# Kernel tuning notes

Hardware: AMD Instinct MI355X
Metric: run time of the kernel (lower is better)

Reference implementation:

```python
import jax, jax.numpy as jnp
import numpy as np

B, L, D, Z, H, N, G = 8, 2048, 1024, 128, 2048, 16, 32
MAXPOS = 2048
EPS = 1e-5
PRIOR_COUNT = 2.0  # TimestepNorm prior pseudo-count


def setup_inputs() -> dict:
    ks = jax.random.split(jax.random.key(0), 12)
    std = 0.02  # bert init
    return {
        "x": jax.random.normal(ks[0], (B, L, D), jnp.float32),
        "prior_mean": jnp.zeros((G,), jnp.float32),
        "prior_logv": jnp.zeros((G,), jnp.float32),
        "tn_weight": jnp.ones((D,), jnp.float32),
        "tn_bias": jnp.zeros((D,), jnp.float32),
        "delta": jax.random.normal(ks[1], (D, N), jnp.float32),
        "alpha": jax.random.normal(ks[2], (D, N), jnp.float32),
        "ema_beta": jax.random.normal(ks[3], (D, N), jnp.float32),
        "ema_gamma": jax.random.normal(ks[4], (D, N), jnp.float32),
        "omega": jax.random.normal(ks[5], (D,), jnp.float32),
        "rms_weight": jnp.ones((D,), jnp.float32),
        "Wv": jax.random.normal(ks[6], (H, D), jnp.float32) * std,
        "bv": jnp.zeros((H,), jnp.float32),
        "Wmx": jax.random.normal(ks[7], (Z + H + 2 * D, D), jnp.float32) * std,
        "bmx": jnp.zeros((Z + H + 2 * D,), jnp.float32),
        "Wh": jax.random.normal(ks[8], (D, H), jnp.float32) * std,
        "qk_gamma": jax.random.normal(ks[9], (2, Z), jnp.float32) * 0.1,
        "qk_beta": jax.random.normal(ks[10], (2, Z), jnp.float32) * 0.1,
        "rel_bias": jax.random.normal(ks[11], (2 * MAXPOS - 1,), jnp.float32) * 0.02,
    }


def timestep_norm(x, prior_mean, prior_logv, weight, bias):
    """Causal cumulative group norm with a prior (TimestepNorm)."""
    m = D // G  # features per group
    xg = x.reshape(B, L, G, m)
    s1 = jnp.cumsum(xg.sum(-1), axis=1)            # B,L,G  running sum
    s2 = jnp.cumsum((xg * xg).sum(-1), axis=1)     # B,L,G  running sum of squares
    cnt = PRIOR_COUNT + m * jnp.arange(1, L + 1, dtype=x.dtype)[None, :, None]
    pv = jnp.exp(prior_logv)
    mean = (PRIOR_COUNT * prior_mean + s1) / cnt
    var = (PRIOR_COUNT * (pv + prior_mean ** 2) + s2) / cnt - mean ** 2
    xn = (xg - mean[..., None]) * jax.lax.rsqrt(var[..., None] + EPS)
    return xn.reshape(B, L, D) * weight + bias


def multihead_ema(x, delta, alpha, ema_beta, ema_gamma, omega):
    """MultiHeadEMA: causal damped-EMA convolution via FFT, plus omega residual."""
    p = jax.nn.sigmoid(delta)                       # D,N
    a = jax.nn.sigmoid(alpha)
    q = 1.0 - p * a                                 # decay in (0,1)
    t = jnp.arange(L, dtype=x.dtype)
    vander = jnp.exp(t[None, None, :] * jnp.log(q)[:, :, None])  # D,N,L
    scale = 1.0 / jnp.sqrt(jnp.asarray(N, x.dtype))
    kern = jnp.einsum('dn,dnl,dn->dl', p * ema_beta, vander, ema_gamma * scale)
    xT = x.transpose(0, 2, 1)                       # B,D,L
    n = 2 * L
    out = jnp.fft.irfft(jnp.fft.rfft(xT, n=n) * jnp.fft.rfft(kern, n=n)[None], n=n)[..., :L]
    out = out + xT * omega[:, None]
    return out.transpose(0, 2, 1)


def _forward(x, prior_mean, prior_logv, tn_weight, tn_bias, delta, alpha,
             ema_beta, ema_gamma, omega, rms_weight, Wv, bv, Wmx, bmx, Wh,
             qk_gamma, qk_beta, rel_bias):
    residual = x
    xn = timestep_norm(x, prior_mean, prior_logv, tn_weight, tn_bias)
    v = jax.nn.silu(xn @ Wv.T + bv)                 # B,L,H
    mx = multihead_ema(xn, delta, alpha, ema_beta, ema_gamma, omega)
    mx = mx * jax.lax.rsqrt(jnp.mean(mx * mx, axis=-1, keepdims=True) + EPS) * rms_weight  # RMSNorm
    base = mx @ Wmx.T + bmx                         # B,L,Z+H+2D
    u = jax.nn.sigmoid(base[..., :D])
    zr = jax.nn.silu(base[..., D:D + Z + H])
    hx = base[..., D + Z + H:]
    z, r = zr[..., :Z], zr[..., Z:]
    zz = z[..., None, :] * qk_gamma + qk_beta       # B,L,2,Z
    q = zz[..., 0, :] * (Z ** -0.5)
    k = zz[..., 1, :]
    # simple relative positional bias: bias[i,j] = rel_bias[MAXPOS-1 + (j-i)]
    idx = (MAXPOS - 1) + (jnp.arange(L)[None, :] - jnp.arange(L)[:, None])
    qk = jnp.einsum('biz,bjz->bij', q, k) + rel_bias[idx]
    causal = jnp.tril(jnp.ones((L, L), bool))
    qk = jnp.where(causal, qk, -jnp.inf)
    attn = jax.nn.softmax(qk, axis=-1)              # B,L,L
    h = jnp.einsum('bij,bjh->bih', attn, v)         # B,L,H
    h = jax.nn.silu(hx + (h * r) @ Wh.T)            # B,L,D
    return residual + u * (h - residual)


def reference(x, prior_mean, prior_logv, tn_weight, tn_bias, delta, alpha,
              ema_beta, ema_gamma, omega, rms_weight, Wv, bv, Wmx, bmx, Wh,
              qk_gamma, qk_beta, rel_bias):
    return _forward(x, prior_mean, prior_logv, tn_weight, tn_bias, delta, alpha,
                    ema_beta, ema_gamma, omega, rms_weight, Wv, bv, Wmx, bmx, Wh,
                    qk_gamma, qk_beta, rel_bias)
```

## Files before the change

kernel.cpp:

```cpp
#include <hip/hip_runtime.h>
#include <stdint.h>

#define B_ 8
#define L_ 2048
#define D_ 1024
#define Z_ 128
#define H_ 2048
#define NE_ 16
#define G_ 32
#define MAXPOS_ 2048
#define NMX_ 4224
#define EPS_ 1e-5f
#define PC_ 2.0f
#define NTILE_ 16
#define NPACK_ 136
#define TILE_ELEMS_ 16384

typedef short bf16x8 __attribute__((ext_vector_type(8)));
typedef float f32x4 __attribute__((ext_vector_type(4)));

__device__ __forceinline__ float bf2f(uint16_t u) {
  union { uint32_t u; float f; } v; v.u = ((uint32_t)u) << 16; return v.f;
}
__device__ __forceinline__ uint16_t f2bf(float f) {
  union { float f; uint32_t u; } v; v.f = f;
  uint32_t r = (v.u + 0x7FFFu + ((v.u >> 16) & 1u)) >> 16;
  return (uint16_t)r;
}
__device__ __forceinline__ float sigmoidf_(float x) { return 1.f / (1.f + __expf(-x)); }
__device__ __forceinline__ float siluf_(float x) { return x / (1.f + __expf(-x)); }

__device__ __forceinline__ float waveRedSum(float v) {
  #pragma unroll
  for (int m = 32; m; m >>= 1) v += __shfl_xor(v, m, 64);
  return v;
}

__device__ __forceinline__ void gl2lds(const uint16_t* g, uint16_t* l) {
  __builtin_amdgcn_global_load_lds(
      (const __attribute__((address_space(1))) void*)g,
      (__attribute__((address_space(3))) void*)l, 16, 0, 0);
}

__global__ __launch_bounds__(256) void k_fallback(float* __restrict__ out, int n, float wsmb) {
  for (int i = blockIdx.x * 256 + threadIdx.x; i < n; i += gridDim.x * 256)
    out[i] = (i == 0) ? wsmb : 0.f;
}

__global__ __launch_bounds__(256) void k_f2bf(const float* __restrict__ src,
                                              uint16_t* __restrict__ dst, int n) {
  for (int i = blockIdx.x * 256 + threadIdx.x; i < n; i += gridDim.x * 256)
    dst[i] = f2bf(src[i]);
}

__global__ __launch_bounds__(256) void k_tnsum(const float* __restrict__ x,
                                               float* __restrict__ s1g,
                                               float* __restrict__ s2g) {
  const int bg = blockIdx.x;
  const int b = bg / G_, g = bg % G_;
  const int tid = threadIdx.x;
  const int j = tid & 31;
  const int lsub = tid >> 5;
  #pragma unroll
  for (int i = 0; i < 16; ++i) {
    const int l = blockIdx.y * 128 + i * 8 + lsub;
    float v = x[((size_t)(b * L_ + l)) * D_ + g * 32 + j];
    float a = v, sq = v * v;
    #pragma unroll
    for (int m = 1; m <= 16; m <<= 1) { a += __shfl_xor(a, m, 64); sq += __shfl_xor(sq, m, 64); }
    if (j == 0) { s1g[(size_t)bg * L_ + l] = a; s2g[(size_t)bg * L_ + l] = sq; }
  }
}

__global__ __launch_bounds__(64) void k_tnscan(float* __restrict__ s1g,
                                               float* __restrict__ s2g) {
  const int bg = blockIdx.x;
  const int lane = threadIdx.x;
  #pragma unroll
  for (int pass = 0; pass < 2; ++pass) {
    float* gp = (pass ? s2g : s1g) + (size_t)bg * L_;
    float loc[32];
    const int b0 = lane * 32;
    float tot = 0.f;
    #pragma unroll
    for (int t = 0; t < 32; ++t) { loc[t] = gp[b0 + t]; tot += loc[t]; }
    float incl = tot;
    #pragma unroll
    for (int off = 1; off < 64; off <<= 1) {
      float nv = __shfl_up(incl, off, 64);
      if (lane >= off) incl += nv;
    }
    float run = incl - tot;
    #pragma unroll
    for (int t = 0; t < 32; ++t) { run += loc[t]; gp[b0 + t] = run; }
  }
}

__global__ __launch_bounds__(256) void k_tnnorm(const float* __restrict__ x,
                                                const float* __restrict__ s1g,
                                                const float* __restrict__ s2g,
                                                const float* __restrict__ pm,
                                                const float* __restrict__ plv,
                                                const float* __restrict__ w,
                                                const float* __restrict__ bias,
                                                uint16_t* __restrict__ xn) {
  const int bg = blockIdx.x;
  const int b = bg / G_, g = bg % G_;
  const int tid = threadIdx.x;
  const int j = tid & 31;
  const int lsub = tid >> 5;
  const float pmv = pm[g];
  const float pvv = __expf(plv[g]);
  const float wj = w[g * 32 + j];
  const float bj = bias[g * 32 + j];
  const float pterm = PC_ * (pvv + pmv * pmv);
  #pragma unroll
  for (int i = 0; i < 16; ++i) {
    const int l = blockIdx.y * 128 + i * 8 + lsub;
    const size_t idx = ((size_t)(b * L_ + l)) * D_ + g * 32 + j;
    const float v = x[idx];
    const float cnt = PC_ + 32.f * (float)(l + 1);
    const float mean = (PC_ * pmv + s1g[(size_t)bg * L_ + l]) / cnt;
    const float var = (pterm + s2g[(size_t)bg * L_ + l]) / cnt - mean * mean;
    xn[idx] = f2bf((v - mean) * rsqrtf(var + EPS_) * wj + bj);
  }
}

template <typename T>
__global__ __launch_bounds__(256) void k_transpose(const T* __restrict__ src,
                                                   T* __restrict__ dst, int R, int C) {
  __shared__ T tile[32][33];
  const size_t batch = (size_t)R * C * blockIdx.z;
  const int c0 = blockIdx.x * 32, r0 = blockIdx.y * 32;
  const int tx = threadIdx.x & 31, ty = threadIdx.x >> 5;
  #pragma unroll
  for (int k = 0; k < 4; ++k) {
    int r = ty + k * 8;
    tile[r][tx] = src[batch + (size_t)(r0 + r) * C + c0 + tx];
  }
  __syncthreads();
  #pragma unroll
  for (int k = 0; k < 4; ++k) {
    int r = ty + k * 8;
    dst[batch + (size_t)(c0 + r) * R + r0 + tx] = tile[tx][r];
  }
}

__global__ __launch_bounds__(64) void k_ema(const uint16_t* __restrict__ xnT,
                                            const float* __restrict__ delta,
                                            const float* __restrict__ alpha,
                                            const float* __restrict__ beta,
                                            const float* __restrict__ gamma,
                                            const float* __restrict__ omega,
                                            float* __restrict__ mxT) {
  __shared__ float hst[64 * NE_];
  const int bd = blockIdx.x;
  const int d = bd & (D_ - 1);
  const int c = threadIdx.x;

  float q[NE_], pb[NE_], gs[NE_];
  #pragma unroll
  for (int n = 0; n < NE_; ++n) {
    float p = sigmoidf_(delta[d * NE_ + n]);
    float a = sigmoidf_(alpha[d * NE_ + n]);
    q[n] = 1.f - p * a;
    pb[n] = p * beta[d * NE_ + n];
    gs[n] = gamma[d * NE_ + n] * 0.25f;
  }

  const uint16_t* xp = xnT + (size_t)bd * L_ + c * 32;
  bf16x8 xin[4];
  #pragma unroll
  for (int s = 0; s < 4; ++s) xin[s] = *(const bf16x8*)(xp + s * 8);

  float h[NE_];
  #pragma unroll
  for (int n = 0; n < NE_; ++n) h[n] = 0.f;

  #pragma unroll
  for (int k = 0; k < 32; ++k) {
    float xv = bf2f((uint16_t)xin[k >> 3][k & 7]);
    #pragma unroll
    for (int n = 0; n < NE_; ++n) h[n] = fmaf(q[n], h[n], pb[n] * xv);
  }
  #pragma unroll
  for (int n = 0; n < NE_; ++n) hst[c * NE_ + n] = h[n];
  __syncthreads();

  if (c < NE_) {
    float qq = q[c];
    float q32 = qq * qq; q32 *= q32; q32 *= q32; q32 *= q32; q32 *= q32;
    float hi = 0.f;
    for (int cc = 0; cc < 64; ++cc) {
      float cur = hst[cc * NE_ + c];
      hst[cc * NE_ + c] = hi;
      hi = fmaf(q32, hi, cur);
    }
  }
  __syncthreads();

  #pragma unroll
  for (int n = 0; n < NE_; ++n) h[n] = hst[c * NE_ + n];
  const float om = omega[d];
  float* op = mxT + (size_t)bd * L_ + c * 32;
  f32x4 ov;
  #pragma unroll
  for (int k = 0; k < 32; ++k) {
    float xv = bf2f((uint16_t)xin[k >> 3][k & 7]);
    float accv = 0.f;
    #pragma unroll
    for (int n = 0; n < NE_; ++n) {
      h[n] = fmaf(q[n], h[n], pb[n] * xv);
      accv = fmaf(gs[n], h[n], accv);
    }
    ov[k & 3] = accv + om * xv;
    if ((k & 3) == 3) *(f32x4*)(op + (k & ~3)) = ov;
  }
}

__global__ __launch_bounds__(256) void k_rms(const float* __restrict__ mx,
                                             const float* __restrict__ w,
                                             uint16_t* __restrict__ mxn) {
  __shared__ float red[4];
  const size_t row = blockIdx.x;
  const int tid = threadIdx.x;
  float ss = 0.f;
  #pragma unroll
  for (int i = 0; i < 4; ++i) {
    float v = mx[row * D_ + tid + i * 256];
    ss += v * v;
  }
  ss = waveRedSum(ss);
  if ((tid & 63) == 0) red[tid >> 6] = ss;
  __syncthreads();
  ss = red[0] + red[1] + red[2] + red[3];
  const float scale = rsqrtf(ss * (1.f / D_) + EPS_);
  #pragma unroll
  for (int i = 0; i < 4; ++i) {
    int dcol = tid + i * 256;
    mxn[row * D_ + dcol] = f2bf(mx[row * D_ + dcol] * scale * w[dcol]);
  }
}

__global__ __launch_bounds__(256) void k_qkprep(const float* __restrict__ z,
                                                const float* __restrict__ qg,
                                                const float* __restrict__ qb,
                                                uint16_t* __restrict__ q,
                                                uint16_t* __restrict__ k, int n) {
  for (int i = blockIdx.x * 256 + threadIdx.x; i < n; i += gridDim.x * 256) {
    int zc = i & (Z_ - 1);
    float v = z[i];
    q[i] = f2bf((v * qg[zc] + qb[zc]) * 0.08838834764831845f);
    k[i] = f2bf(v * qg[Z_ + zc] + qb[Z_ + zc]);
  }
}

template <int MODE>
__global__ __launch_bounds__(256) void k_gemm(
    const uint16_t* __restrict__ A, const uint16_t* __restrict__ Bm,
    int N, int K,
    const float* __restrict__ bias,
    float* __restrict__ outf, uint16_t* __restrict__ outb,
    uint16_t* __restrict__ ubuf, float* __restrict__ zbuf,
    uint16_t* __restrict__ rbuf, float* __restrict__ hxbuf,
    const float* __restrict__ x0) {
  const int bm = blockIdx.x * 128;
  const int bn = blockIdx.y * 128;
  __shared__ uint16_t As[128 * 32];
  __shared__ uint16_t Bs[128 * 32];
  const int tid = threadIdx.x;
  const int wave = tid >> 6, lane = tid & 63;
  const int quad = lane >> 4, r16 = lane & 15;
  const int wm = wave >> 1, wn = wave & 1;
  const int rowW = wm * 64, colW = wn * 64;

  f32x4 acc[4][4];
  const f32x4 zf = {0.f, 0.f, 0.f, 0.f};
  #pragma unroll
  for (int i = 0; i < 4; ++i)
    #pragma unroll
    for (int j = 0; j < 4; ++j) acc[i][j] = zf;

  const int rA = tid >> 2;
  const int sg = (tid & 3) * 8;
  const uint16_t* gA0 = A + (size_t)(bm + rA) * K + sg;
  const uint16_t* gA1 = A + (size_t)(bm + 64 + rA) * K + sg;
  const uint16_t* gB0 = Bm + (size_t)(bn + rA) * K + sg;
  const uint16_t* gB1 = Bm + (size_t)(bn + 64 + rA) * K + sg;
  uint16_t* lA0 = As + tid * 8;
  uint16_t* lA1 = As + 2048 + tid * 8;
  uint16_t* lB0 = Bs + tid * 8;
  uint16_t* lB1 = Bs + 2048 + tid * 8;

  for (int kb = 0; kb < K; kb += 32) {
    __syncthreads();
    gl2lds(gA0 + kb, lA0);
    gl2lds(gA1 + kb, lA1);
    gl2lds(gB0 + kb, lB0);
    gl2lds(gB1 + kb, lB1);
    __syncthreads();
    bf16x8 af[4], bfr[4];
    #pragma unroll
    for (int i = 0; i < 4; ++i)
      af[i] = *(const bf16x8*)&As[(rowW + i * 16 + r16) * 32 + quad * 8];
    #pragma unroll
    for (int j = 0; j < 4; ++j)
      bfr[j] = *(const bf16x8*)&Bs[(colW + j * 16 + r16) * 32 + quad * 8];
    #pragma unroll
    for (int i = 0; i < 4; ++i)
      #pragma unroll
      for (int j = 0; j < 4; ++j)
        acc[i][j] = __builtin_amdgcn_mfma_f32_16x16x32_bf16(af[i], bfr[j], acc[i][j], 0, 0, 0);
  }

  #pragma unroll
  for (int i = 0; i < 4; ++i) {
    #pragma unroll
    for (int j = 0; j < 4; ++j) {
      #pragma unroll
      for (int r = 0; r < 4; ++r) {
        const int row = bm + rowW + i * 16 + quad * 4 + r;
        const int col = bn + colW + j * 16 + r16;
        float val = acc[i][j][r];
        if (MODE == 0) {
          outb[(size_t)row * N + col] = f2bf(siluf_(val + bias[col]));
        } else if (MODE == 1) {
          val += bias[col];
          if (col < D_)                 ubuf[(size_t)row * D_ + col] = f2bf(sigmoidf_(val));
          else if (col < D_ + Z_)       zbuf[(size_t)row * Z_ + (col - D_)] = siluf_(val);
          else if (col < D_ + Z_ + H_)  rbuf[(size_t)row * H_ + (col - D_ - Z_)] = f2bf(siluf_(val));
          else                          hxbuf[(size_t)row * D_ + (col - D_ - Z_ - H_)] = val;
        } else {
          const size_t idx = (size_t)row * N + col;
          float g = siluf_(val + hxbuf[idx]);
          float xv = x0[idx];
          outf[idx] = xv + bf2f(ubuf[idx]) * (g - xv);
        }
      }
    }
  }
}

__global__ __launch_bounds__(256) void k_qksm(
    const uint16_t* __restrict__ qg, const uint16_t* __restrict__ kg,
    const float* __restrict__ relb, uint16_t* __restrict__ Pp) {
  __shared__ uint16_t Ks[128 * 128];
  __shared__ float relwin[256];
  const int qt = blockIdx.x;
  const int bl = blockIdx.y;
  const int tid = threadIdx.x;
  const int w = tid >> 6, lane = tid & 63;
  const int quad = lane >> 4, r16 = lane & 15;
  const uint16_t* qb_b = qg + (size_t)bl * L_ * Z_;
  const uint16_t* kb_b = kg + (size_t)bl * L_ * Z_;
  uint16_t* P_b = Pp + (size_t)bl * NPACK_ * TILE_ELEMS_;

  bf16x8 aq[2][4];
  #pragma unroll
  for (int i = 0; i < 2; ++i)
    #pragma unroll
    for (int s = 0; s < 4; ++s)
      aq[i][s] = *(const bf16x8*)&qb_b[(size_t)(qt * 128 + w * 32 + i * 16 + r16) * Z_ +
                                       s * 32 + quad * 8];

  float m8[8], l8[8];
  #pragma unroll
  for (int t = 0; t < 8; ++t) { m8[t] = -3.4e38f; l8[t] = 0.f; }

  const f32x4 zf = {0.f, 0.f, 0.f, 0.f};

  for (int kt = 0; kt <= qt; ++kt) {
    __syncthreads();
    const uint16_t* src = kb_b + (size_t)kt * 128 * Z_;
    #pragma unroll
    for (int s2 = 0; s2 < 8; ++s2)
      gl2lds(src + s2 * 2048 + tid * 8, Ks + s2 * 2048 + tid * 8);
    if (tid < 255) relwin[tid] = relb[2047 + (kt - qt) * 128 - 127 + tid];
    __syncthreads();
    #pragma unroll
    for (int j = 0; j < 8; ++j) {
      f32x4 a0 = zf, a1 = zf;
      #pragma unroll
      for (int s = 0; s < 4; ++s) {
        bf16x8 bk = *(const bf16x8*)&Ks[(j * 16 + r16) * 128 + s * 32 + quad * 8];
        a0 = __builtin_amdgcn_mfma_f32_16x16x32_bf16(aq[0][s], bk, a0, 0, 0, 0);
        a1 = __builtin_amdgcn_mfma_f32_16x16x32_bf16(aq[1][s], bk, a1, 0, 0, 0);
      }
      #pragma unroll
      for (int i = 0; i < 2; ++i) {
        const f32x4 av = i ? a1 : a0;
        #pragma unroll
        for (int r = 0; r < 4; ++r) {
          const int rloc = w * 32 + i * 16 + quad * 4 + r;
          const int cloc = j * 16 + r16;
          if (kt < qt || cloc <= rloc) {
            const float v = av[r] + relwin[cloc - rloc + 127];
            const int t = i * 4 + r;
            const float mn = fmaxf(m8[t], v);
            l8[t] = l8[t] * __expf(m8[t] - mn) + __expf(v - mn);
            m8[t] = mn;
          }
        }
      }
    }
  }

  #pragma unroll
  for (int t = 0; t < 8; ++t) {
    #pragma unroll
    for (int msk = 1; msk <= 8; msk <<= 1) {
      const float mo = __shfl_xor(m8[t], msk, 64);
      const float lo = __shfl_xor(l8[t], msk, 64);
      const float mn = fmaxf(m8[t], mo);
      l8[t] = l8[t] * __expf(m8[t] - mn) + lo * __expf(mo - mn);
      m8[t] = mn;
    }
    l8[t] = 1.f / l8[t];
  }

  for (int kt = 0; kt <= qt; ++kt) {
    __syncthreads();
    const uint16_t* src = kb_b + (size_t)kt * 128 * Z_;
    #pragma unroll
    for (int s2 = 0; s2 < 8; ++s2)
      gl2lds(src + s2 * 2048 + tid * 8, Ks + s2 * 2048 + tid * 8);
    if (tid < 255) relwin[tid] = relb[2047 + (kt - qt) * 128 - 127 + tid];
    __syncthreads();
    uint16_t* Pt = P_b + (size_t)(qt * (qt + 1) / 2 + kt) * TILE_ELEMS_;
    #pragma unroll
    for (int j = 0; j < 8; ++j) {
      f32x4 a0 = zf, a1 = zf;
      #pragma unroll
      for (int s = 0; s < 4; ++s) {
        bf16x8 bk = *(const bf16x8*)&Ks[(j * 16 + r16) * 128 + s * 32 + quad * 8];
        a0 = __builtin_amdgcn_mfma_f32_16x16x32_bf16(aq[0][s], bk, a0, 0, 0, 0);
        a1 = __builtin_amdgcn_mfma_f32_16x16x32_bf16(aq[1][s], bk, a1, 0, 0, 0);
      }
      #pragma unroll
      for (int i = 0; i < 2; ++i) {
        const f32x4 av = i ? a1 : a0;
        #pragma unroll
        for (int r = 0; r < 4; ++r) {
          const int rloc = w * 32 + i * 16 + quad * 4 + r;
          const int cloc = j * 16 + r16;
          const int t = i * 4 + r;
          float p = 0.f;
          if (kt < qt || cloc <= rloc) {
            const float v = av[r] + relwin[cloc - rloc + 127];
            p = __expf(v - m8[t]) * l8[t];
          }
          Pt[rloc * 128 + cloc] = f2bf(p);
        }
      }
    }
  }
}

__global__ __launch_bounds__(256) void k_pv(
    const uint16_t* __restrict__ Pp, const uint16_t* __restrict__ vT,
    uint16_t* __restrict__ rh) {
  __shared__ uint16_t As[128 * 32];
  __shared__ uint16_t Bs[128 * 32];
  const int qt = blockIdx.x;
  const int bn = blockIdx.y * 128;
  const int bl = blockIdx.z;
  const uint16_t* P_b = Pp + (size_t)bl * NPACK_ * TILE_ELEMS_;
  const uint16_t* v_b = vT + (size_t)bl * H_ * L_;
  uint16_t* rh_b = rh + (size_t)bl * L_ * H_;

  const int tid = threadIdx.x;
  const int wave = tid >> 6, lane = tid & 63;
  const int quad = lane >> 4, r16 = lane & 15;
  const int wm = wave >> 1, wn = wave & 1;
  const int rowW = wm * 64, colW = wn * 64;

  f32x4 acc[4][4];
  const f32x4 zf = {0.f, 0.f, 0.f, 0.f};
  #pragma unroll
  for (int i = 0; i < 4; ++i)
    #pragma unroll
    for (int j = 0; j < 4; ++j) acc[i][j] = zf;

  const int rA = tid >> 2;
  const int sg = (tid & 3) * 8;
  uint16_t* lA0 = As + tid * 8;
  uint16_t* lA1 = As + 2048 + tid * 8;
  uint16_t* lB0 = Bs + tid * 8;
  uint16_t* lB1 = Bs + 2048 + tid * 8;

  for (int kt = 0; kt <= qt; ++kt) {
    const uint16_t* At = P_b + (size_t)(qt * (qt + 1) / 2 + kt) * TILE_ELEMS_;
    #pragma unroll
    for (int ks = 0; ks < 4; ++ks) {
      const int kb = kt * 128 + ks * 32;
      __syncthreads();
      gl2lds(At + rA * 128 + ks * 32 + sg, lA0);
      gl2lds(At + (rA + 64) * 128 + ks * 32 + sg, lA1);
      gl2lds(v_b + (size_t)(bn + rA) * L_ + kb + sg, lB0);
      gl2lds(v_b + (size_t)(bn + 64 + rA) * L_ + kb + sg, lB1);
      __syncthreads();
      bf16x8 af[4], bfr[4];
      #pragma unroll
      for (int i = 0; i < 4; ++i)
        af[i] = *(const bf16x8*)&As[(rowW + i * 16 + r16) * 32 + quad * 8];
      #pragma unroll
      for (int j = 0; j < 4; ++j)
        bfr[j] = *(const bf16x8*)&Bs[(colW + j * 16 + r16) * 32 + quad * 8];
      #pragma unroll
      for (int i = 0; i < 4; ++i)
        #pragma unroll
        for (int j = 0; j < 4; ++j)
          acc[i][j] = __builtin_amdgcn_mfma_f32_16x16x32_bf16(af[i], bfr[j], acc[i][j], 0, 0, 0);
    }
  }

  #pragma unroll
  for (int i = 0; i < 4; ++i) {
    #pragma unroll
    for (int j = 0; j < 4; ++j) {
      #pragma unroll
      for (int r = 0; r < 4; ++r) {
        const int row = qt * 128 + rowW + i * 16 + quad * 4 + r;
        const int col = bn + colW + j * 16 + r16;
        const size_t idx = (size_t)row * H_ + col;
        const float rv = bf2f(rh_b[idx]);
        rh_b[idx] = f2bf(acc[i][j][r] * rv);
      }
    }
  }
}

extern "C" void kernel_launch(void* const* d_in, const int* in_sizes, int n_in,
                              void* d_out, int out_size, void* d_ws, size_t ws_size,
                              hipStream_t stream) {
  (void)in_sizes; (void)n_in;
  const float* x         = (const float*)d_in[0];
  const float* prior_mean= (const float*)d_in[1];
  const float* prior_logv= (const float*)d_in[2];
  const float* tn_w      = (const float*)d_in[3];
  const float* tn_b      = (const float*)d_in[4];
  const float* delta     = (const float*)d_in[5];
  const float* alpha     = (const float*)d_in[6];
  const float* ema_beta  = (const float*)d_in[7];
  const float* ema_gamma = (const float*)d_in[8];
  const float* omega     = (const float*)d_in[9];
  const float* rms_w     = (const float*)d_in[10];
  const float* Wv        = (const float*)d_in[11];
  const float* bv        = (const float*)d_in[12];
  const float* Wmx       = (const float*)d_in[13];
  const float* bmx       = (const float*)d_in[14];
  const float* Wh        = (const float*)d_in[15];
  const float* qk_gamma  = (const float*)d_in[16];
  const float* qk_beta   = (const float*)d_in[17];
  const float* rel_bias  = (const float*)d_in[18];
  float* out = (float*)d_out;

  const int BL = B_ * L_;
  const size_t MB = 1024 * 1024;
  const size_t REQUIRED = 256 * MB;

  if (ws_size < REQUIRED) {
    k_fallback<<<dim3(4096), dim3(256), 0, stream>>>(out, out_size, (float)(ws_size / MB));
    return;
  }

  char* p = (char*)d_ws;
  uint16_t* xn   = (uint16_t*)(p);
  uint16_t* ubuf = (uint16_t*)(p);
  float*    s1g  = (float*)   (p + 32 * MB);
  float*    s2g  = (float*)   (p + 34 * MB);
  uint16_t* xnT  = (uint16_t*)(p + 32 * MB);
  uint16_t* mxn  = (uint16_t*)(p + 32 * MB);
  uint16_t* vbuf = (uint16_t*)(p + 64 * MB);
  float*    mx   = (float*)   (p + 64 * MB);
  uint16_t* rbuf = (uint16_t*)(p + 64 * MB);
  uint16_t* wv_b = (uint16_t*)(p + 128 * MB);
  uint16_t* vT   = (uint16_t*)(p + 128 * MB);
  uint16_t* wmx_b = (uint16_t*)(p + 192 * MB);
  uint16_t* wh_b  = (uint16_t*)(p + 192 * MB);
  float*    zb    = (float*)   (p + 201 * MB);
  uint16_t* qb    = (uint16_t*)(p + 209 * MB);
  uint16_t* kb2   = (uint16_t*)(p + 213 * MB);
  uint16_t* Ppack = (uint16_t*)(p + 217 * MB);
  float* mxT = out;
  float* hx  = out;

  k_f2bf<<<dim3(1024), dim3(256), 0, stream>>>(Wv, wv_b, H_ * D_);
  k_f2bf<<<dim3(2048), dim3(256), 0, stream>>>(Wmx, wmx_b, NMX_ * D_);
  k_tnsum<<<dim3(B_ * G_, 16), dim3(256), 0, stream>>>(x, s1g, s2g);
  k_tnscan<<<dim3(B_ * G_), dim3(64), 0, stream>>>(s1g, s2g);
  k_tnnorm<<<dim3(B_ * G_, 16), dim3(256), 0, stream>>>(
      x, s1g, s2g, prior_mean, prior_logv, tn_w, tn_b, xn);
  k_transpose<uint16_t><<<dim3(D_ / 32, L_ / 32, B_), dim3(256), 0, stream>>>(xn, xnT, L_, D_);
  k_gemm<0><<<dim3(BL / 128, H_ / 128), dim3(256), 0, stream>>>(
      xn, wv_b, H_, D_, bv, nullptr, vbuf,
      nullptr, nullptr, nullptr, nullptr, nullptr);
  k_transpose<uint16_t><<<dim3(H_ / 32, L_ / 32, B_), dim3(256), 0, stream>>>(vbuf, vT, L_, H_);
  k_ema<<<dim3(B_ * D_), dim3(64), 0, stream>>>(xnT, delta, alpha, ema_beta, ema_gamma, omega, mxT);
  k_transpose<float><<<dim3(L_ / 32, D_ / 32, B_), dim3(256), 0, stream>>>(mxT, mx, D_, L_);
  k_rms<<<dim3(BL), dim3(256), 0, stream>>>(mx, rms_w, mxn);
  k_gemm<1><<<dim3(BL / 128, NMX_ / 128), dim3(256), 0, stream>>>(
      mxn, wmx_b, NMX_, D_, bmx, nullptr, nullptr,
      ubuf, zb, rbuf, hx, nullptr);
  k_qkprep<<<dim3(1024), dim3(256), 0, stream>>>(zb, qk_gamma, qk_beta, qb, kb2, BL * Z_);
  k_qksm<<<dim3(NTILE_, B_), dim3(256), 0, stream>>>(qb, kb2, rel_bias, Ppack);
  k_pv<<<dim3(NTILE_, H_ / 128, B_), dim3(256), 0, stream>>>(Ppack, vT, rbuf);
  k_f2bf<<<dim3(1024), dim3(256), 0, stream>>>(Wh, wh_b, D_ * H_);
  k_gemm<4><<<dim3(BL / 128, D_ / 128), dim3(256), 0, stream>>>(
      rbuf, wh_b, D_, H_, nullptr, out, nullptr,
      ubuf, nullptr, nullptr, hx, x);
}
```

Before: 1.315 ms.

## Replace 128x128 GEMM with double-buffered 256x256 tiled GEMM using swizzled LDS

The three dense GEMMs move from a 128x128 tile, single-buffered, K=32 kernel to a 512-thread 256x256 tile kernel. The new kernel double-buffers 64-wide K slices in LDS, prefetches the next slice while the MFMAs run, XOR-swizzles the LDS layout to avoid bank conflicts, remaps workgroup IDs across chiplets, and raises wave priority around the MFMA bursts. The Wmx weight is zero-padded to 4352 rows so the fused projection divides evenly into 256-wide tiles, and the epilogue skips the padded columns. The aim is more data reuse per tile and overlap of global loads with compute. The costs are higher register and LDS use (128 KB LDS) and fewer workgroups in flight for the smaller GEMMs.

After: 1.605 ms. +22.0%, slower.

```diff
diff --git a/kernel.cpp b/kernel.cpp
--- a/kernel.cpp
+++ b/kernel.cpp
@@ -10,6 +10,7 @@
 #define G_ 32
 #define MAXPOS_ 2048
 #define NMX_ 4224
+#define NMXP_ 4352
 #define EPS_ 1e-5f
 #define PC_ 2.0f
 #define NTILE_ 16
@@ -42,6 +43,12 @@
       (__attribute__((address_space(3))) void*)l, 16, 0, 0);
 }
 
+__device__ __forceinline__ void barrier_mem() {
+  asm volatile("" ::: "memory");
+  __builtin_amdgcn_s_barrier();
+  asm volatile("" ::: "memory");
+}
+
 __global__ __launch_bounds__(256) void k_fallback(float* __restrict__ out, int n, float wsmb) {
   for (int i = blockIdx.x * 256 + threadIdx.x; i < n; i += gridDim.x * 256)
     out[i] = (i == 0) ? wsmb : 0.f;
@@ -51,6 +58,12 @@
                                               uint16_t* __restrict__ dst, int n) {
   for (int i = blockIdx.x * 256 + threadIdx.x; i < n; i += gridDim.x * 256)
     dst[i] = f2bf(src[i]);
+}
+
+__global__ __launch_bounds__(256) void k_f2bf_pad(const float* __restrict__ src,
+                                                  uint16_t* __restrict__ dst, int n, int ntot) {
+  for (int i = blockIdx.x * 256 + threadIdx.x; i < ntot; i += gridDim.x * 256)
+    dst[i] = (i < n) ? f2bf(src[i]) : (uint16_t)0;
 }
 
 __global__ __launch_bounds__(256) void k_tnsum(const float* __restrict__ x,
@@ -255,8 +268,41 @@
   }
 }
 
+
+#define STG(c, kh, kb, MAT) do {                                              \
+    const uint16_t* _g = ((MAT) ? gB : gA) + (kb) + (kh) * 32;                \
+    uint16_t* _l = sm + (c) * 32768 + (MAT) * 16384 + (kh) * 8192 + t * 8;    \
+    gl2lds(_g, _l); gl2lds(_g + rsk, _l + 4096);                              \
+  } while (0)
+
+#define LDA4(c, kh, ih) do {                                                  \
+    _Pragma("unroll")                                                         \
+    for (int _i = 0; _i < 4; ++_i)                                            \
+      af[_i] = *(const bf16x8*)&sm[(c) * 32768 + (kh) * 8192 + aOff +         \
+                                   ((ih) * 4 + _i) * 512];                    \
+  } while (0)
+
+#define LDB4(c, kh) do {                                                      \
+    _Pragma("unroll")                                                         \
+    for (int _j = 0; _j < 4; ++_j)                                            \
+      bfr[_j] = *(const bf16x8*)&sm[(c) * 32768 + (kh) * 8192 + bOff +        \
+                                    _j * 512];                                \
+  } while (0)
+
+#define MM16(ih) do {                                                         \
+    __builtin_amdgcn_s_setprio(1);                                            \
+    _Pragma("unroll")                                                         \
+    for (int _i = 0; _i < 4; ++_i) {                                          \
+      _Pragma("unroll")                                                       \
+      for (int _j = 0; _j < 4; ++_j)                                          \
+        acc[(ih) * 4 + _i][_j] = __builtin_amdgcn_mfma_f32_16x16x32_bf16(     \
+            af[_i], bfr[_j], acc[(ih) * 4 + _i][_j], 0, 0, 0);                \
+    }                                                                         \
+    __builtin_amdgcn_s_setprio(0);                                            \
+  } while (0)
+
 template <int MODE>
-__global__ __launch_bounds__(256) void k_gemm(
+__global__ __launch_bounds__(512, 2) void k_gemm256(
     const uint16_t* __restrict__ A, const uint16_t* __restrict__ Bm,
     int N, int K,
     const float* __restrict__ bias,
@@ -264,72 +310,88 @@
     uint16_t* __restrict__ ubuf, float* __restrict__ zbuf,
     uint16_t* __restrict__ rbuf, float* __restrict__ hxbuf,
     const float* __restrict__ x0) {
-  const int bm = blockIdx.x * 128;
-  const int bn = blockIdx.y * 128;
-  __shared__ uint16_t As[128 * 32];
-  __shared__ uint16_t Bs[128 * 32];
-  const int tid = threadIdx.x;
-  const int wave = tid >> 6, lane = tid & 63;
+  __shared__ uint16_t sm[65536];
+  const int t = threadIdx.x;
+  const int lane = t & 63, wave = t >> 6;
   const int quad = lane >> 4, r16 = lane & 15;
-  const int wm = wave >> 1, wn = wave & 1;
-  const int rowW = wm * 64, colW = wn * 64;
-
-  f32x4 acc[4][4];
+  const int wm = wave >> 2, wn = wave & 3;
+
+  const int nbx = gridDim.x;
+  const int nwg = nbx * gridDim.y;
+  int lid = blockIdx.y * nbx + blockIdx.x;
+  const int cpx = nwg >> 3;
+  lid = (lid & 7) * cpx + (lid >> 3);
+  const int bm = (lid % nbx) * 256;
+  const int bn = (lid / nbx) * 256;
+
+  f32x4 acc[8][4];
   const f32x4 zf = {0.f, 0.f, 0.f, 0.f};
   #pragma unroll
-  for (int i = 0; i < 4; ++i)
+  for (int i = 0; i < 8; ++i)
     #pragma unroll
     for (int j = 0; j < 4; ++j) acc[i][j] = zf;
 
-  const int rA = tid >> 2;
-  const int sg = (tid & 3) * 8;
-  const uint16_t* gA0 = A + (size_t)(bm + rA) * K + sg;
-  const uint16_t* gA1 = A + (size_t)(bm + 64 + rA) * K + sg;
-  const uint16_t* gB0 = Bm + (size_t)(bn + rA) * K + sg;
-  const uint16_t* gB1 = Bm + (size_t)(bn + 64 + rA) * K + sg;
-  uint16_t* lA0 = As + tid * 8;
-  uint16_t* lA1 = As + 2048 + tid * 8;
-  uint16_t* lB0 = Bs + tid * 8;
-  uint16_t* lB1 = Bs + 2048 + tid * 8;
-
-  for (int kb = 0; kb < K; kb += 32) {
-    __syncthreads();
-    gl2lds(gA0 + kb, lA0);
-    gl2lds(gA1 + kb, lA1);
-    gl2lds(gB0 + kb, lB0);
-    gl2lds(gB1 + kb, lB1);
-    __syncthreads();
-    bf16x8 af[4], bfr[4];
-    #pragma unroll
-    for (int i = 0; i < 4; ++i)
-      af[i] = *(const bf16x8*)&As[(rowW + i * 16 + r16) * 32 + quad * 8];
-    #pragma unroll
-    for (int j = 0; j < 4; ++j)
-      bfr[j] = *(const bf16x8*)&Bs[(colW + j * 16 + r16) * 32 + quad * 8];
-    #pragma unroll
-    for (int i = 0; i < 4; ++i)
-      #pragma unroll
-      for (int j = 0; j < 4; ++j)
-        acc[i][j] = __builtin_amdgcn_mfma_f32_16x16x32_bf16(af[i], bfr[j], acc[i][j], 0, 0, 0);
-  }
-
-  #pragma unroll
-  for (int i = 0; i < 4; ++i) {
+  const int srow = t >> 2;
+  const int sg = (((t & 3) ^ ((t >> 4) & 3)) << 3);
+  const uint16_t* gA = A + (size_t)(bm + srow) * K + sg;
+  const uint16_t* gB = Bm + (size_t)(bn + srow) * K + sg;
+  const size_t rsk = (size_t)128 * K;
+
+  const int G8 = (quad ^ ((r16 >> 2) & 3)) << 3;
+  const int aOff = (wm * 128 + r16) * 32 + G8;
+  const int bOff = 16384 + (wn * 64 + r16) * 32 + G8;
+
+  const int NT = K >> 6;
+
+  STG(0, 0, 0, 0); STG(0, 0, 0, 1); STG(0, 1, 0, 0); STG(0, 1, 0, 1);
+  asm volatile("s_waitcnt vmcnt(4)" ::: "memory");
+  barrier_mem();
+
+  bf16x8 af[4], bfr[4];
+  for (int tt = 0; tt < NT; ++tt) {
+    const int c = tt & 1, cn = c ^ 1;
+    const int kbn = (tt + 1) << 6;
+    const bool pf = (tt + 1 < NT);
+    LDA4(c, 0, 0); LDB4(c, 0);
+    if (pf) STG(cn, 0, kbn, 0);
+    MM16(0);
+    barrier_mem();
+    LDA4(c, 0, 1);
+    if (pf) STG(cn, 0, kbn, 1);
+    MM16(1);
+    if (pf) asm volatile("s_waitcnt vmcnt(4)" ::: "memory");
+    else    asm volatile("s_waitcnt vmcnt(0)" ::: "memory");
+    barrier_mem();
+    LDA4(c, 1, 0); LDB4(c, 1);
+    if (pf) STG(cn, 1, kbn, 0);
+    MM16(0);
+    barrier_mem();
+    LDA4(c, 1, 1);
+    if (pf) STG(cn, 1, kbn, 1);
+    MM16(1);
+    if (pf) asm volatile("s_waitcnt vmcnt(4)" ::: "memory");
+    barrier_mem();
+  }
+
+  #pragma unroll
+  for (int gi = 0; gi < 8; ++gi) {
     #pragma unroll
     for (int j = 0; j < 4; ++j) {
       #pragma unroll
       for (int r = 0; r < 4; ++r) {
-        const int row = bm + rowW + i * 16 + quad * 4 + r;
-        const int col = bn + colW + j * 16 + r16;
-        float val = acc[i][j][r];
+        const int row = bm + wm * 128 + gi * 16 + quad * 4 + r;
+        const int col = bn + wn * 64 + j * 16 + r16;
+        float val = acc[gi][j][r];
         if (MODE == 0) {
           outb[(size_t)row * N + col] = f2bf(siluf_(val + bias[col]));
         } else if (MODE == 1) {
-          val += bias[col];
-          if (col < D_)                 ubuf[(size_t)row * D_ + col] = f2bf(sigmoidf_(val));
-          else if (col < D_ + Z_)       zbuf[(size_t)row * Z_ + (col - D_)] = siluf_(val);
-          else if (col < D_ + Z_ + H_)  rbuf[(size_t)row * H_ + (col - D_ - Z_)] = f2bf(siluf_(val));
-          else                          hxbuf[(size_t)row * D_ + (col - D_ - Z_ - H_)] = val;
+          if (col < NMX_) {
+            val += bias[col];
+            if (col < D_)                 ubuf[(size_t)row * D_ + col] = f2bf(sigmoidf_(val));
+            else if (col < D_ + Z_)       zbuf[(size_t)row * Z_ + (col - D_)] = siluf_(val);
+            else if (col < D_ + Z_ + H_)  rbuf[(size_t)row * H_ + (col - D_ - Z_)] = f2bf(siluf_(val));
+            else                          hxbuf[(size_t)row * D_ + (col - D_ - Z_ - H_)] = val;
+          }
         } else {
           const size_t idx = (size_t)row * N + col;
           float g = siluf_(val + hxbuf[idx]);
@@ -340,6 +402,11 @@
     }
   }
 }
+
+#undef STG
+#undef LDA4
+#undef LDB4
+#undef MM16
 
 __global__ __launch_bounds__(256) void k_qksm(
     const uint16_t* __restrict__ qg, const uint16_t* __restrict__ kg,
@@ -586,27 +653,27 @@
   float* hx  = out;
 
   k_f2bf<<<dim3(1024), dim3(256), 0, stream>>>(Wv, wv_b, H_ * D_);
-  k_f2bf<<<dim3(2048), dim3(256), 0, stream>>>(Wmx, wmx_b, NMX_ * D_);
+  k_f2bf_pad<<<dim3(2048), dim3(256), 0, stream>>>(Wmx, wmx_b, NMX_ * D_, NMXP_ * D_);
   k_tnsum<<<dim3(B_ * G_, 16), dim3(256), 0, stream>>>(x, s1g, s2g);
   k_tnscan<<<dim3(B_ * G_), dim3(64), 0, stream>>>(s1g, s2g);
   k_tnnorm<<<dim3(B_ * G_, 16), dim3(256), 0, stream>>>(
       x, s1g, s2g, prior_mean, prior_logv, tn_w, tn_b, xn);
   k_transpose<uint16_t><<<dim3(D_ / 32, L_ / 32, B_), dim3(256), 0, stream>>>(xn, xnT, L_, D_);
-  k_gemm<0><<<dim3(BL / 128, H_ / 128), dim3(256), 0, stream>>>(
+  k_gemm256<0><<<dim3(BL / 256, H_ / 256), dim3(512), 0, stream>>>(
       xn, wv_b, H_, D_, bv, nullptr, vbuf,
       nullptr, nullptr, nullptr, nullptr, nullptr);
   k_transpose<uint16_t><<<dim3(H_ / 32, L_ / 32, B_), dim3(256), 0, stream>>>(vbuf, vT, L_, H_);
   k_ema<<<dim3(B_ * D_), dim3(64), 0, stream>>>(xnT, delta, alpha, ema_beta, ema_gamma, omega, mxT);
   k_transpose<float><<<dim3(L_ / 32, D_ / 32, B_), dim3(256), 0, stream>>>(mxT, mx, D_, L_);
   k_rms<<<dim3(BL), dim3(256), 0, stream>>>(mx, rms_w, mxn);
-  k_gemm<1><<<dim3(BL / 128, NMX_ / 128), dim3(256), 0, stream>>>(
-      mxn, wmx_b, NMX_, D_, bmx, nullptr, nullptr,
+  k_gemm256<1><<<dim3(BL / 256, NMXP_ / 256), dim3(512), 0, stream>>>(
+      mxn, wmx_b, NMXP_, D_, bmx, nullptr, nullptr,
       ubuf, zb, rbuf, hx, nullptr);
   k_qkprep<<<dim3(1024), dim3(256), 0, stream>>>(zb, qk_gamma, qk_beta, qb, kb2, BL * Z_);
   k_qksm<<<dim3(NTILE_, B_), dim3(256), 0, stream>>>(qb, kb2, rel_bias, Ppack);
   k_pv<<<dim3(NTILE_, H_ / 128, B_), dim3(256), 0, stream>>>(Ppack, vT, rbuf);
   k_f2bf<<<dim3(1024), dim3(256), 0, stream>>>(Wh, wh_b, D_ * H_);
-  k_gemm<4><<<dim3(BL / 128, D_ / 128), dim3(256), 0, stream>>>(
+  k_gemm256<4><<<dim3(BL / 256, D_ / 256), dim3(512), 0, stream>>>(
       rbuf, wh_b, D_, H_, nullptr, out, nullptr,
       ubuf, nullptr, nullptr, hx, x);
 }
```

## Replace 128x128 GEMM with double-buffered 256x256 tile kernel using 512 threads

Applied to the files above, without the earlier changes.

Replaces the 128x128, single-buffered, K=32 GEMM with a 256x256 tile GEMM on 512 threads (8 waves) with K=64 steps. It double-buffers global-to-LDS loads in 128 KB of shared memory so the next tile loads during the current MFMAs. The Wmx weight is zero-padded to 4352 rows so the N dimension divides evenly by 256, and the epilogue skips the padded columns. The aim is more operand reuse per byte loaded and fewer stalls between load and compute. The cost is higher register and LDS pressure, fewer blocks per CU, and wasted work on the padded rows.

After: 1.273 ms. 1.03x faster.

```diff
diff --git a/kernel.cpp b/kernel.cpp
--- a/kernel.cpp
+++ b/kernel.cpp
@@ -10,6 +10,7 @@
 #define G_ 32
 #define MAXPOS_ 2048
 #define NMX_ 4224
+#define NMXP_ 4352
 #define EPS_ 1e-5f
 #define PC_ 2.0f
 #define NTILE_ 16
@@ -51,6 +52,12 @@
                                               uint16_t* __restrict__ dst, int n) {
   for (int i = blockIdx.x * 256 + threadIdx.x; i < n; i += gridDim.x * 256)
     dst[i] = f2bf(src[i]);
+}
+
+__global__ __launch_bounds__(256) void k_f2bf_pad(const float* __restrict__ src,
+                                                  uint16_t* __restrict__ dst, int n, int ntot) {
+  for (int i = blockIdx.x * 256 + threadIdx.x; i < ntot; i += gridDim.x * 256)
+    dst[i] = (i < n) ? f2bf(src[i]) : (uint16_t)0;
 }
 
 __global__ __launch_bounds__(256) void k_tnsum(const float* __restrict__ x,
@@ -255,8 +262,9 @@
   }
 }
 
+
 template <int MODE>
-__global__ __launch_bounds__(256) void k_gemm(
+__global__ __launch_bounds__(512, 2) void k_gemm256(
     const uint16_t* __restrict__ A, const uint16_t* __restrict__ Bm,
     int N, int K,
     const float* __restrict__ bias,
@@ -264,72 +272,89 @@
     uint16_t* __restrict__ ubuf, float* __restrict__ zbuf,
     uint16_t* __restrict__ rbuf, float* __restrict__ hxbuf,
     const float* __restrict__ x0) {
-  const int bm = blockIdx.x * 128;
-  const int bn = blockIdx.y * 128;
-  __shared__ uint16_t As[128 * 32];
-  __shared__ uint16_t Bs[128 * 32];
-  const int tid = threadIdx.x;
-  const int wave = tid >> 6, lane = tid & 63;
+  __shared__ uint16_t sm[65536];
+  const int t = threadIdx.x;
+  const int lane = t & 63, wave = t >> 6;
   const int quad = lane >> 4, r16 = lane & 15;
-  const int wm = wave >> 1, wn = wave & 1;
-  const int rowW = wm * 64, colW = wn * 64;
-
-  f32x4 acc[4][4];
+  const int wm = wave >> 2, wn = wave & 3;
+  const int bm = blockIdx.x * 256;
+  const int bn = blockIdx.y * 256;
+
+  f32x4 acc[8][4];
   const f32x4 zf = {0.f, 0.f, 0.f, 0.f};
   #pragma unroll
-  for (int i = 0; i < 4; ++i)
+  for (int i = 0; i < 8; ++i)
     #pragma unroll
     for (int j = 0; j < 4; ++j) acc[i][j] = zf;
 
-  const int rA = tid >> 2;
-  const int sg = (tid & 3) * 8;
-  const uint16_t* gA0 = A + (size_t)(bm + rA) * K + sg;
-  const uint16_t* gA1 = A + (size_t)(bm + 64 + rA) * K + sg;
-  const uint16_t* gB0 = Bm + (size_t)(bn + rA) * K + sg;
-  const uint16_t* gB1 = Bm + (size_t)(bn + 64 + rA) * K + sg;
-  uint16_t* lA0 = As + tid * 8;
-  uint16_t* lA1 = As + 2048 + tid * 8;
-  uint16_t* lB0 = Bs + tid * 8;
-  uint16_t* lB1 = Bs + 2048 + tid * 8;
-
-  for (int kb = 0; kb < K; kb += 32) {
+  const uint16_t* gA = A + (size_t)(bm + (t >> 3)) * K + (t & 7) * 8;
+  const uint16_t* gB = Bm + (size_t)(bn + (t >> 3)) * K + (t & 7) * 8;
+  const size_t qstep = (size_t)64 * K;
+  uint16_t* lA = sm + t * 8;
+  uint16_t* lB = sm + 16384 + t * 8;
+
+  const int aBase = (wm * 128 + r16) * 64 + quad * 8;
+  const int bBase = 16384 + (wn * 64 + r16) * 64 + quad * 8;
+
+#define STAGE(c, kb) do {                                                     \
+    _Pragma("unroll")                                                         \
+    for (int q = 0; q < 4; ++q) {                                             \
+      gl2lds(gA + q * qstep + (kb), lA + (c) * 32768 + q * 4096);             \
+      gl2lds(gB + q * qstep + (kb), lB + (c) * 32768 + q * 4096);             \
+    }                                                                         \
+  } while (0)
+
+  const int NT = K >> 6;
+
+  STAGE(0, 0);
+  __syncthreads();
+
+  bf16x8 af[4], bfr[4];
+  for (int tt = 0; tt < NT; ++tt) {
+    const int c = tt & 1;
+    const int co = c * 32768;
+    if (tt + 1 < NT) STAGE(c ^ 1, (tt + 1) * 64);
+    #pragma unroll
+    for (int kh = 0; kh < 2; ++kh) {
+      #pragma unroll
+      for (int ih = 0; ih < 2; ++ih) {
+        #pragma unroll
+        for (int i = 0; i < 4; ++i)
+          af[i] = *(const bf16x8*)&sm[co + aBase + (ih * 4 + i) * 1024 + kh * 32];
+        #pragma unroll
+        for (int j = 0; j < 4; ++j)
+          bfr[j] = *(const bf16x8*)&sm[co + bBase + j * 1024 + kh * 32];
+        #pragma unroll
+        for (int i = 0; i < 4; ++i)
+          #pragma unroll
+          for (int j = 0; j < 4; ++j)
+            acc[ih * 4 + i][j] = __builtin_amdgcn_mfma_f32_16x16x32_bf16(
+                af[i], bfr[j], acc[ih * 4 + i][j], 0, 0, 0);
+      }
+    }
     __syncthreads();
-    gl2lds(gA0 + kb, lA0);
-    gl2lds(gA1 + kb, lA1);
-    gl2lds(gB0 + kb, lB0);
-    gl2lds(gB1 + kb, lB1);
-    __syncthreads();
-    bf16x8 af[4], bfr[4];
-    #pragma unroll
-    for (int i = 0; i < 4; ++i)
-      af[i] = *(const bf16x8*)&As[(rowW + i * 16 + r16) * 32 + quad * 8];
-    #pragma unroll
-    for (int j = 0; j < 4; ++j)
-      bfr[j] = *(const bf16x8*)&Bs[(colW + j * 16 + r16) * 32 + quad * 8];
-    #pragma unroll
-    for (int i = 0; i < 4; ++i)
-      #pragma unroll
-      for (int j = 0; j < 4; ++j)
-        acc[i][j] = __builtin_amdgcn_mfma_f32_16x16x32_bf16(af[i], bfr[j], acc[i][j], 0, 0, 0);
-  }
-
-  #pragma unroll
-  for (int i = 0; i < 4; ++i) {
+  }
+#undef STAGE
+
+  #pragma unroll
+  for (int gi = 0; gi < 8; ++gi) {
     #pragma unroll
     for (int j = 0; j < 4; ++j) {
       #pragma unroll
       for (int r = 0; r < 4; ++r) {
-        const int row = bm + rowW + i * 16 + quad * 4 + r;
-        const int col = bn + colW + j * 16 + r16;
-        float val = acc[i][j][r];
+        const int row = bm + wm * 128 + gi * 16 + quad * 4 + r;
+        const int col = bn + wn * 64 + j * 16 + r16;
+        float val = acc[gi][j][r];
         if (MODE == 0) {
           outb[(size_t)row * N + col] = f2bf(siluf_(val + bias[col]));
         } else if (MODE == 1) {
-          val += bias[col];
-          if (col < D_)                 ubuf[(size_t)row * D_ + col] = f2bf(sigmoidf_(val));
-          else if (col < D_ + Z_)       zbuf[(size_t)row * Z_ + (col - D_)] = siluf_(val);
-          else if (col < D_ + Z_ + H_)  rbuf[(size_t)row * H_ + (col - D_ - Z_)] = f2bf(siluf_(val));
-          else                          hxbuf[(size_t)row * D_ + (col - D_ - Z_ - H_)] = val;
+          if (col < NMX_) {
+            val += bias[col];
+            if (col < D_)                 ubuf[(size_t)row * D_ + col] = f2bf(sigmoidf_(val));
+            else if (col < D_ + Z_)       zbuf[(size_t)row * Z_ + (col - D_)] = siluf_(val);
+            else if (col < D_ + Z_ + H_)  rbuf[(size_t)row * H_ + (col - D_ - Z_)] = f2bf(siluf_(val));
+            else                          hxbuf[(size_t)row * D_ + (col - D_ - Z_ - H_)] = val;
+          }
         } else {
           const size_t idx = (size_t)row * N + col;
           float g = siluf_(val + hxbuf[idx]);
@@ -586,27 +611,27 @@
   float* hx  = out;
 
   k_f2bf<<<dim3(1024), dim3(256), 0, stream>>>(Wv, wv_b, H_ * D_);
-  k_f2bf<<<dim3(2048), dim3(256), 0, stream>>>(Wmx, wmx_b, NMX_ * D_);
+  k_f2bf_pad<<<dim3(2048), dim3(256), 0, stream>>>(Wmx, wmx_b, NMX_ * D_, NMXP_ * D_);
   k_tnsum<<<dim3(B_ * G_, 16), dim3(256), 0, stream>>>(x, s1g, s2g);
   k_tnscan<<<dim3(B_ * G_), dim3(64), 0, stream>>>(s1g, s2g);
   k_tnnorm<<<dim3(B_ * G_, 16), dim3(256), 0, stream>>>(
       x, s1g, s2g, prior_mean, prior_logv, tn_w, tn_b, xn);
   k_transpose<uint16_t><<<dim3(D_ / 32, L_ / 32, B_), dim3(256), 0, stream>>>(xn, xnT, L_, D_);
-  k_gemm<0><<<dim3(BL / 128, H_ / 128), dim3(256), 0, stream>>>(
+  k_gemm256<0><<<dim3(BL / 256, H_ / 256), dim3(512), 0, stream>>>(
       xn, wv_b, H_, D_, bv, nullptr, vbuf,
       nullptr, nullptr, nullptr, nullptr, nullptr);
   k_transpose<uint16_t><<<dim3(H_ / 32, L_ / 32, B_), dim3(256), 0, stream>>>(vbuf, vT, L_, H_);
   k_ema<<<dim3(B_ * D_), dim3(64), 0, stream>>>(xnT, delta, alpha, ema_beta, ema_gamma, omega, mxT);
   k_transpose<float><<<dim3(L_ / 32, D_ / 32, B_), dim3(256), 0, stream>>>(mxT, mx, D_, L_);
   k_rms<<<dim3(BL), dim3(256), 0, stream>>>(mx, rms_w, mxn);
-  k_gemm<1><<<dim3(BL / 128, NMX_ / 128), dim3(256), 0, stream>>>(
-      mxn, wmx_b, NMX_, D_, bmx, nullptr, nullptr,
+  k_gemm256<1><<<dim3(BL / 256, NMXP_ / 256), dim3(512), 0, stream>>>(
+      mxn, wmx_b, NMXP_, D_, bmx, nullptr, nullptr,
       ubuf, zb, rbuf, hx, nullptr);
   k_qkprep<<<dim3(1024), dim3(256), 0, stream>>>(zb, qk_gamma, qk_beta, qb, kb2, BL * Z_);
   k_qksm<<<dim3(NTILE_, B_), dim3(256), 0, stream>>>(qb, kb2, rel_bias, Ppack);
   k_pv<<<dim3(NTILE_, H_ / 128, B_), dim3(256), 0, stream>>>(Ppack, vT, rbuf);
   k_f2bf<<<dim3(1024), dim3(256), 0, stream>>>(Wh, wh_b, D_ * H_);
-  k_gemm<4><<<dim3(BL / 128, D_ / 128), dim3(256), 0, stream>>>(
+  k_gemm256<4><<<dim3(BL / 256, D_ / 256), dim3(512), 0, stream>>>(
       rbuf, wh_b, D_, H_, nullptr, out, nullptr,
       ubuf, nullptr, nullptr, hx, x);
 }
```
